# Kernel optimization log

Measured on AMD Instinct MI355X. Metric: run time of the kernel, lower is better.

## Reference

```python
import jax, jax.numpy as jnp
import numpy as np

N = 100000      # nodes
E = 1600000     # edges (avg degree 16)
NFEAT = 128
NHID = 128
NOUT = 1
BN_EPS = 1e-5


def setup_inputs() -> dict:
    key = jax.random.key(0)
    ks = jax.random.split(key, 8)
    s = 0.05  # weight scale for numerical stability through relu stack
    return {
        "x": jax.random.normal(ks[0], (N, NFEAT), jnp.float32),
        "edge_index": jax.random.randint(ks[1], (2, E), 0, N, dtype=jnp.int64),
        "edge_weight": jax.random.uniform(ks[2], (E,), jnp.float32),
        "conv1_W": jax.random.normal(ks[3], (NFEAT, NHID), jnp.float32) * s,
        "conv1_b": jnp.zeros((NHID,), jnp.float32),
        "conv2_W": jax.random.normal(ks[4], (NHID, NHID), jnp.float32) * s,
        "conv2_b": jnp.zeros((NHID,), jnp.float32),
        "bn1_gamma": jnp.ones((NHID,), jnp.float32),
        "bn1_beta": jnp.zeros((NHID,), jnp.float32),
        "bn2_gamma": jnp.ones((NHID,), jnp.float32),
        "bn2_beta": jnp.zeros((NHID,), jnp.float32),
        "fc1_W": jax.random.normal(ks[5], (NFEAT + 2 * NHID, NHID), jnp.float32) * s,
        "fc1_b": jnp.zeros((NHID,), jnp.float32),
        "fc2_W": jax.random.normal(ks[6], (NHID, NOUT), jnp.float32) * s,
        "fc2_b": jnp.zeros((NOUT,), jnp.float32),
    }


def _gcn_norm(edge_index, edge_weight, num_nodes):
    # PyG gcn_norm: add self-loops (weight 1), symmetric D^-1/2 A D^-1/2.
    row, col = edge_index[0], edge_index[1]
    loop = jnp.arange(num_nodes, dtype=row.dtype)
    rows = jnp.concatenate([row, loop])
    cols = jnp.concatenate([col, loop])
    w = jnp.concatenate([edge_weight, jnp.ones((num_nodes,), edge_weight.dtype)])
    deg = jax.ops.segment_sum(w, cols, num_segments=num_nodes)
    dinv = jnp.where(deg > 0, jax.lax.rsqrt(deg), 0.0)
    norm = dinv[rows] * w * dinv[cols]
    return rows, cols, norm


def _gcn_conv(x, rows, cols, norm, W, b, num_nodes):
    h = x @ W                                  # [N, out]
    msg = h[rows] * norm[:, None]              # gather + scale  [E+N, out]
    out = jax.ops.segment_sum(msg, cols, num_segments=num_nodes)  # scatter-add
    return out + b


def _bn(x, gamma, beta):
    # BatchNorm1d, training-mode batch statistics (biased variance)
    m = jnp.mean(x, axis=0)
    v = jnp.var(x, axis=0)
    return (x - m) * jax.lax.rsqrt(v + BN_EPS) * gamma + beta


def reference(x, edge_index, edge_weight, conv1_W, conv1_b, conv2_W, conv2_b,
              bn1_gamma, bn1_beta, bn2_gamma, bn2_beta,
              fc1_W, fc1_b, fc2_W, fc2_b):
    n = x.shape[0]
    rows, cols, norm = _gcn_norm(edge_index, edge_weight, n)
    h0 = x
    h1 = jax.nn.relu(_gcn_conv(h0, rows, cols, norm, conv1_W, conv1_b, n))
    h1 = _bn(h1, bn1_gamma, bn1_beta)          # dropout p=0 -> identity
    h2 = jax.nn.relu(_gcn_conv(h1, rows, cols, norm, conv2_W, conv2_b, n))
    h2 = _bn(h2, bn2_gamma, bn2_beta)
    cat = jnp.concatenate([h0, h1, h2], axis=1)   # [N, nfeat+2*nhid]
    z = jax.nn.relu(cat @ fc1_W + fc1_b)
    z = jax.nn.relu(z @ fc2_W + fc2_b)
    return z.reshape(-1)
```

## Files before the change

### kernel.cpp

```cpp
#include <hip/hip_runtime.h>

typedef __attribute__((ext_vector_type(8))) short short8;
typedef __attribute__((ext_vector_type(4))) float f32x4;

constexpr int N = 100000;
constexpr int E = 1600000;
constexpr int F = 128;
constexpr float EPS = 1e-5f;
constexpr int NB = (N + 1023) / 1024;

constexpr int R_RNG = 16;
constexpr int BINS = 6250;
constexpr int G2 = 64;
constexpr int NPB = 640;
constexpr int EPB = E / NPB;
constexpr int EPB4 = EPB / 4;

__device__ __forceinline__ short bf16hi(float v) {
  unsigned u = __float_as_uint(v);
  unsigned r = (u + 0x7fffu + ((u >> 16) & 1u)) >> 16;
  return (short)r;
}
__device__ __forceinline__ float bf16f(short h) {
  return __uint_as_float(((unsigned)(unsigned short)h) << 16);
}
__device__ __forceinline__ float bflo(unsigned v) {
  return __uint_as_float(v << 16);
}
__device__ __forceinline__ float bfhi(unsigned v) {
  return __uint_as_float(v & 0xffff0000u);
}

__global__ __launch_bounds__(256) void k_phist(const int* __restrict__ ei, int* __restrict__ Psl) {
  __shared__ int h16[16];
  const int b = blockIdx.x;
  const int tid = threadIdx.x;
  if (tid < 16) h16[tid] = 0;
  __syncthreads();
  const int4* cols4 = (const int4*)(ei + E);
  for (int t = tid; t < EPB4; t += 256) {
    int4 c = cols4[b * EPB4 + t];
    atomicAdd(&h16[c.x / BINS], 1);
    atomicAdd(&h16[c.y / BINS], 1);
    atomicAdd(&h16[c.z / BINS], 1);
    atomicAdd(&h16[c.w / BINS], 1);
  }
  __syncthreads();
  if (tid == 0) {
    int run = 0;
#pragma unroll
    for (int r = 0; r < 16; ++r) { Psl[b * 17 + r] = run; run += h16[r]; }
    Psl[b * 17 + 16] = run;
  }
}

__global__ __launch_bounds__(256) void k_pscatter(const int* __restrict__ ei, const float* __restrict__ ew,
                                                  const int* __restrict__ Psl, int2* __restrict__ pe) {
  __shared__ int cur[16];
  const int b = blockIdx.x;
  const int tid = threadIdx.x;
  if (tid < 16) cur[tid] = Psl[b * 17 + tid];
  __syncthreads();
  const int4* cols4 = (const int4*)(ei + E);
  const int4* rows4 = (const int4*)ei;
  const float4* ew4 = (const float4*)ew;
  const int base = b * EPB;
  for (int t = tid; t < EPB4; t += 256) {
    int4 c = cols4[b * EPB4 + t];
    int4 rr = rows4[b * EPB4 + t];
    float4 w = ew4[b * EPB4 + t];
#pragma unroll
    for (int j = 0; j < 4; ++j) {
      int cc = (j == 0) ? c.x : (j == 1) ? c.y : (j == 2) ? c.z : c.w;
      int rv = (j == 0) ? rr.x : (j == 1) ? rr.y : (j == 2) ? rr.z : rr.w;
      float wv = (j == 0) ? w.x : (j == 1) ? w.y : (j == 2) ? w.z : w.w;
      int r = cc / BINS;
      int pos = base + atomicAdd(&cur[r], 1);
      pe[pos] = make_int2((rv << 13) | (cc - r * BINS), __float_as_int(wv));
    }
  }
}

__global__ __launch_bounds__(256) void k_hist2(const int2* __restrict__ pe, const int* __restrict__ Psl,
                                               int* __restrict__ P) {
  __shared__ int hist[BINS];
  const int r = blockIdx.x / G2;
  const int g = blockIdx.x % G2;
  const int tid = threadIdx.x;
  for (int i = tid; i < BINS; i += 256) hist[i] = 0;
  __syncthreads();
  for (int b = g; b < NPB; b += G2) {
    const int s = Psl[b * 17 + r], e2 = Psl[b * 17 + r + 1];
    const int eb = b * EPB;
    for (int t = s + tid; t < e2; t += 256)
      atomicAdd(&hist[pe[eb + t].x & 0x1FFF], 1);
  }
  __syncthreads();
  for (int i = tid; i < BINS; i += 256) P[(size_t)blockIdx.x * BINS + i] = hist[i];
}

__global__ __launch_bounds__(256) void k_reduce(int* __restrict__ P, int* __restrict__ cnt) {
  int b = blockIdx.x * 256 + threadIdx.x;
  if (b >= N) return;
  int r = b / BINS, lb = b % BINS;
  size_t base = (size_t)r * G2 * BINS + lb;
  int run = 0;
#pragma unroll 4
  for (int g = 0; g < G2; ++g) {
    size_t idx = base + (size_t)g * BINS;
    int v = P[idx];
    P[idx] = run;
    run += v;
  }
  cnt[b] = run;
}

__global__ __launch_bounds__(256) void k_bsum(const int* __restrict__ cnt, int* __restrict__ bsum) {
  __shared__ int sh[256];
  int base = blockIdx.x * 1024 + threadIdx.x * 4;
  int s = 0;
  if (base + 3 < N) {
    int4 v = *(const int4*)&cnt[base];
    s = v.x + v.y + v.z + v.w;
  } else {
#pragma unroll
    for (int j = 0; j < 4; ++j)
      if (base + j < N) s += cnt[base + j];
  }
  sh[threadIdx.x] = s;
  __syncthreads();
  for (int o = 128; o > 0; o >>= 1) {
    if (threadIdx.x < o) sh[threadIdx.x] += sh[threadIdx.x + o];
    __syncthreads();
  }
  if (threadIdx.x == 0) bsum[blockIdx.x] = sh[0];
}

__global__ __launch_bounds__(128) void k_bscan(const int* __restrict__ bsum, int* __restrict__ bbase,
                                               int* __restrict__ offN) {
  __shared__ int sh[128];
  const int t = threadIdx.x;
  int v = (t < NB) ? bsum[t] : 0;
  sh[t] = v;
  __syncthreads();
  for (int o = 1; o < 128; o <<= 1) {
    int u = (t >= o) ? sh[t - o] : 0;
    __syncthreads();
    sh[t] += u;
    __syncthreads();
  }
  if (t < NB) bbase[t] = sh[t] - v;
  if (t == 127) *offN = sh[127];
}

__global__ __launch_bounds__(256) void k_off(const int* __restrict__ cnt, const int* __restrict__ bbase,
                                             int* __restrict__ off) {
  __shared__ int sh[256];
  int base = blockIdx.x * 1024 + threadIdx.x * 4;
  int c[4] = {0, 0, 0, 0};
  if (base + 3 < N) {
    int4 v = *(const int4*)&cnt[base];
    c[0] = v.x; c[1] = v.y; c[2] = v.z; c[3] = v.w;
  } else {
#pragma unroll
    for (int j = 0; j < 4; ++j)
      if (base + j < N) c[j] = cnt[base + j];
  }
  int s = c[0] + c[1] + c[2] + c[3];
  sh[threadIdx.x] = s;
  __syncthreads();
  for (int o = 1; o < 256; o <<= 1) {
    int u = (threadIdx.x >= o) ? sh[threadIdx.x - o] : 0;
    __syncthreads();
    sh[threadIdx.x] += u;
    __syncthreads();
  }
  int run = bbase[blockIdx.x] + sh[threadIdx.x] - s;
#pragma unroll
  for (int j = 0; j < 4; ++j) {
    if (base + j < N) { off[base + j] = run; run += c[j]; }
  }
}

__global__ __launch_bounds__(256) void k_scatter3(const int2* __restrict__ pe, const int* __restrict__ Psl,
                                                  const int* __restrict__ off, const int* __restrict__ P,
                                                  int2* __restrict__ cpair) {
  __shared__ int base[BINS];
  const int r = blockIdx.x / G2;
  const int g = blockIdx.x % G2;
  const int tid = threadIdx.x;
  for (int i = tid; i < BINS; i += 256)
    base[i] = off[r * BINS + i] + P[(size_t)blockIdx.x * BINS + i];
  __syncthreads();
  for (int b = g; b < NPB; b += G2) {
    const int s = Psl[b * 17 + r], e2 = Psl[b * 17 + r + 1];
    const int eb = b * EPB;
    for (int t = s + tid; t < e2; t += 256) {
      int2 p = pe[eb + t];
      int pos = atomicAdd(&base[p.x & 0x1FFF], 1);
      cpair[pos] = make_int2((int)(((unsigned)p.x) >> 13), p.y);
    }
  }
}

__global__ __launch_bounds__(256) void k_degcsc(const int2* __restrict__ cpair, const int* __restrict__ off,
                                                float* __restrict__ dinv) {
  int i = blockIdx.x * 256 + threadIdx.x;
  if (i >= N) return;
  int b = off[i], e2 = off[i + 1];
  float s = 1.0f;
  for (int p = b; p < e2; ++p) s += __int_as_float(cpair[p].y);
  dinv[i] = rsqrtf(s);
}

__global__ __launch_bounds__(256) void k_nrm(const int* __restrict__ off,
                                             const float* __restrict__ dinv, int2* __restrict__ cpair) {
  int i = blockIdx.x * 256 + threadIdx.x;
  if (i >= N) return;
  int b = off[i], e2 = off[i + 1];
  float di = dinv[i];
  for (int p = b; p < e2; ++p) {
    int2 cp = cpair[p];
    cpair[p].y = __float_as_int(dinv[cp.x] * __int_as_float(cp.y) * di);
  }
}

__global__ __launch_bounds__(256) void k_wprep_all(
    const float* __restrict__ W1, const float* __restrict__ W2, const float* __restrict__ Wf1,
    short* __restrict__ wt1h, short* __restrict__ wt1l,
    short* __restrict__ wt2h, short* __restrict__ wt2l,
    short* __restrict__ wtfh, short* __restrict__ wtfl,
    float* __restrict__ st1, float* __restrict__ st2) {
  int idx = blockIdx.x * 256 + threadIdx.x;
  if (idx < 256) st1[idx] = 0.f;
  else if (idx < 512) st2[idx - 256] = 0.f;
  const float* W;
  short *wh, *wl;
  int K, li;
  if (idx < 16384)      { W = W1;  wh = wt1h; wl = wt1l; K = 128; li = idx; }
  else if (idx < 32768) { W = W2;  wh = wt2h; wl = wt2l; K = 128; li = idx - 16384; }
  else if (idx < 81920) { W = Wf1; wh = wtfh; wl = wtfl; K = 384; li = idx - 32768; }
  else return;
  int k = li >> 7, c = li & 127;
  float v = W[(size_t)k * 128 + c];
  short h = bf16hi(v);
  short l = bf16hi(v - bf16f(h));
  wh[(size_t)c * K + k] = h;
  wl[(size_t)c * K + k] = l;
}

__global__ void k_bnparam(const float* __restrict__ st, const float* __restrict__ gamma,
                          const float* __restrict__ beta, float* __restrict__ p) {
  int t = threadIdx.x;
  if (t >= 128) return;
  const float inv_n = 1.0f / (float)N;
  float m = st[t] * inv_n;
  float var = fmaf(-m, m, st[128 + t] * inv_n);
  float sc = gamma[t] * rsqrtf(var + EPS);
  p[t] = sc;
  p[128 + t] = fmaf(-m, sc, beta[t]);
}

template <int KSTEPS, bool OBF16, bool FC2>
__global__ __launch_bounds__(256) void k_gemm_mfma(
    const float* __restrict__ a0, const float* __restrict__ p0,
    const float* __restrict__ a1, const float* __restrict__ p1,
    const float* __restrict__ a2, const float* __restrict__ p2,
    const short* __restrict__ wth, const short* __restrict__ wtl,
    const float* __restrict__ bias, void* __restrict__ Cout,
    const float* __restrict__ wf2, const float* __restrict__ bf2) {
  constexpr int KT = KSTEPS * 32;
  __shared__ short Ah[128][40];
  __shared__ short Al[128][40];
  __shared__ short Bh[128][40];
  __shared__ short Bl[128][40];
  __shared__ float red[2][128];

  const int tid = threadIdx.x;
  const int m0 = blockIdx.x * 128;
  const int sr = tid >> 1;
  const int sk = (tid & 1) * 16;
  const int arow = min(m0 + sr, N - 1);
  const int lane = tid & 63;
  const int lr = lane & 15;
  const int lg = lane >> 4;
  const int wv = tid >> 6;
  const int wr = wv >> 1;
  const int wc = wv & 1;

  f32x4 acc[4][4];
#pragma unroll
  for (int m = 0; m < 4; ++m)
#pragma unroll
    for (int n = 0; n < 4; ++n) acc[m][n] = (f32x4){0.f, 0.f, 0.f, 0.f};

  for (int ks = 0; ks < KSTEPS; ++ks) {
    const int seg = ks >> 2;
    const int koff = (ks & 3) * 32;
    const float* __restrict__ A = (seg == 0) ? a0 : ((seg == 1) ? a1 : a2);
    const float* __restrict__ P = (seg == 0) ? p0 : ((seg == 1) ? p1 : p2);

    const float4* src = (const float4*)(A + (size_t)arow * F + koff + sk);
    float v[16];
#pragma unroll
    for (int q = 0; q < 4; ++q) {
      float4 t = src[q];
      v[q * 4 + 0] = t.x; v[q * 4 + 1] = t.y; v[q * 4 + 2] = t.z; v[q * 4 + 3] = t.w;
    }
    if (P) {
      const int c0 = koff + sk;
#pragma unroll
      for (int q = 0; q < 4; ++q) {
        float4 s = *(const float4*)&P[c0 + q * 4];
        float4 b = *(const float4*)&P[128 + c0 + q * 4];
        v[q * 4 + 0] = fmaf(v[q * 4 + 0], s.x, b.x);
        v[q * 4 + 1] = fmaf(v[q * 4 + 1], s.y, b.y);
        v[q * 4 + 2] = fmaf(v[q * 4 + 2], s.z, b.z);
        v[q * 4 + 3] = fmaf(v[q * 4 + 3], s.w, b.w);
      }
    }
    short hh[16], ll[16];
#pragma unroll
    for (int j = 0; j < 16; ++j) {
      hh[j] = bf16hi(v[j]);
      ll[j] = bf16hi(v[j] - bf16f(hh[j]));
    }

    __syncthreads();

    short8 t0, t1, u0, u1;
#pragma unroll
    for (int j = 0; j < 8; ++j) { t0[j] = hh[j]; t1[j] = hh[8 + j]; u0[j] = ll[j]; u1[j] = ll[8 + j]; }
    *(short8*)&Ah[sr][sk] = t0;
    *(short8*)&Ah[sr][sk + 8] = t1;
    *(short8*)&Al[sr][sk] = u0;
    *(short8*)&Al[sr][sk + 8] = u1;

    const size_t wbase = (size_t)sr * KT + ks * 32 + sk;
    *(short8*)&Bh[sr][sk]     = *(const short8*)&wth[wbase];
    *(short8*)&Bh[sr][sk + 8] = *(const short8*)&wth[wbase + 8];
    *(short8*)&Bl[sr][sk]     = *(const short8*)&wtl[wbase];
    *(short8*)&Bl[sr][sk + 8] = *(const short8*)&wtl[wbase + 8];

    __syncthreads();

    short8 afh[4], afl[4], bfh[4], bfl[4];
#pragma unroll
    for (int m = 0; m < 4; ++m) {
      const int r2 = wr * 64 + m * 16 + lr;
      afh[m] = *(const short8*)&Ah[r2][lg * 8];
      afl[m] = *(const short8*)&Al[r2][lg * 8];
    }
#pragma unroll
    for (int n = 0; n < 4; ++n) {
      const int c2 = wc * 64 + n * 16 + lr;
      bfh[n] = *(const short8*)&Bh[c2][lg * 8];
      bfl[n] = *(const short8*)&Bl[c2][lg * 8];
    }
#pragma unroll
    for (int m = 0; m < 4; ++m)
#pragma unroll
      for (int n = 0; n < 4; ++n) {
        acc[m][n] = __builtin_amdgcn_mfma_f32_16x16x32_bf16(afh[m], bfh[n], acc[m][n], 0, 0, 0);
        acc[m][n] = __builtin_amdgcn_mfma_f32_16x16x32_bf16(afl[m], bfh[n], acc[m][n], 0, 0, 0);
        acc[m][n] = __builtin_amdgcn_mfma_f32_16x16x32_bf16(afh[m], bfl[n], acc[m][n], 0, 0, 0);
      }
  }

  float bv[4];
#pragma unroll
  for (int n = 0; n < 4; ++n) bv[n] = bias ? bias[wc * 64 + n * 16 + lr] : 0.f;

  if (FC2) {
    float w2v[4];
#pragma unroll
    for (int n = 0; n < 4; ++n) w2v[n] = wf2[wc * 64 + n * 16 + lr];
#pragma unroll
    for (int m = 0; m < 4; ++m) {
#pragma unroll
      for (int j = 0; j < 4; ++j) {
        float partial = 0.f;
#pragma unroll
        for (int n = 0; n < 4; ++n)
          partial += fmaxf(acc[m][n][j] + bv[n], 0.f) * w2v[n];
#pragma unroll
        for (int o = 8; o >= 1; o >>= 1) partial += __shfl_xor(partial, o, 16);
        if (lr == 0) red[wc][wr * 64 + m * 16 + lg * 4 + j] = partial;
      }
    }
    __syncthreads();
    if (tid < 128) {
      const int row = m0 + tid;
      if (row < N) {
        float s = red[0][tid] + red[1][tid] + bf2[0];
        ((float*)Cout)[row] = fmaxf(s, 0.f);
      }
    }
  } else {
#pragma unroll
    for (int m = 0; m < 4; ++m) {
#pragma unroll
      for (int j = 0; j < 4; ++j) {
        const int row = m0 + wr * 64 + m * 16 + lg * 4 + j;
        if (row < N) {
#pragma unroll
          for (int n = 0; n < 4; ++n) {
            const int col = wc * 64 + n * 16 + lr;
            float o = acc[m][n][j] + bv[n];
            if (bias) o = fmaxf(o, 0.f);
            if (OBF16) {
              ((unsigned short*)Cout)[(size_t)row * F + col] = (unsigned short)bf16hi(o);
            } else {
              ((float*)Cout)[(size_t)row * F + col] = o;
            }
          }
        }
      }
    }
  }
}

__global__ __launch_bounds__(256) void k_agg(
    const unsigned* __restrict__ h,
    const int2* __restrict__ cpair, const int* __restrict__ off,
    const float* __restrict__ dinv, const float* __restrict__ bias,
    float* __restrict__ out) {
  const int i = blockIdx.x * 4 + (threadIdx.x >> 6);
  if (i >= N) return;
  const int lane = threadIdx.x & 63;
  const float di = dinv[i];
  unsigned sv = h[(size_t)i * 64 + lane];
  float acc0 = di * di * bflo(sv);
  float acc1 = di * di * bfhi(sv);
  int e = off[i];
  const int eend = off[i + 1];
  for (; e + 8 <= eend; e += 8) {
    int2 cp[8];
    unsigned vv[8];
#pragma unroll
    for (int j = 0; j < 8; ++j) cp[j] = cpair[e + j];
#pragma unroll
    for (int j = 0; j < 8; ++j) vv[j] = h[(size_t)cp[j].x * 64 + lane];
#pragma unroll
    for (int j = 0; j < 8; ++j) {
      float w = __int_as_float(cp[j].y);
      acc0 = fmaf(w, bflo(vv[j]), acc0);
      acc1 = fmaf(w, bfhi(vv[j]), acc1);
    }
  }
  for (; e < eend; ++e) {
    int2 cp = cpair[e];
    float w = __int_as_float(cp.y);
    unsigned v = h[(size_t)cp.x * 64 + lane];
    acc0 = fmaf(w, bflo(v), acc0);
    acc1 = fmaf(w, bfhi(v), acc1);
  }
  float2 b = *(const float2*)&bias[lane * 2];
  float2 o = make_float2(fmaxf(acc0 + b.x, 0.f), fmaxf(acc1 + b.y, 0.f));
  *(float2*)&out[(size_t)i * F + lane * 2] = o;
}

__global__ __launch_bounds__(256) void k_stats(const float* __restrict__ h, float* __restrict__ sums) {
  const int col = threadIdx.x & 127;
  const int half = threadIdx.x >> 7;
  float s = 0.f, s2 = 0.f;
  for (int r = blockIdx.x * 2 + half; r < N; r += gridDim.x * 2) {
    float v = h[(size_t)r * F + col];
    s += v;
    s2 = fmaf(v, v, s2);
  }
  __shared__ float sh[256];
  sh[threadIdx.x] = s;
  __syncthreads();
  if (half == 0) atomicAdd(&sums[col], s + sh[col + 128]);
  __syncthreads();
  sh[threadIdx.x] = s2;
  __syncthreads();
  if (half == 0) atomicAdd(&sums[128 + col], s2 + sh[col + 128]);
}

extern "C" void kernel_launch(void* const* d_in, const int* in_sizes, int n_in,
                              void* d_out, int out_size, void* d_ws, size_t ws_size,
                              hipStream_t stream) {
  const float* x   = (const float*)d_in[0];
  const int*   ei  = (const int*)d_in[1];
  const float* ew  = (const float*)d_in[2];
  const float* W1  = (const float*)d_in[3];
  const float* b1  = (const float*)d_in[4];
  const float* W2  = (const float*)d_in[5];
  const float* b2  = (const float*)d_in[6];
  const float* g1  = (const float*)d_in[7];
  const float* be1 = (const float*)d_in[8];
  const float* g2  = (const float*)d_in[9];
  const float* be2 = (const float*)d_in[10];
  const float* Wf1 = (const float*)d_in[11];
  const float* bf1 = (const float*)d_in[12];
  const float* Wf2 = (const float*)d_in[13];
  const float* bf2 = (const float*)d_in[14];
  float* out = (float*)d_out;

  char* p = (char*)d_ws;
  auto take = [&](size_t bytes) {
    char* r = p;
    p += (bytes + 255) & ~(size_t)255;
    return r;
  };
  float* st1  = (float*)take(256 * 4);
  float* st2  = (float*)take(256 * 4);
  int*   cnt  = (int*)take((size_t)N * 4);
  int*   off  = (int*)take((size_t)(N + 1) * 4);
  int*   bsum = (int*)take((size_t)NB * 4);
  int*   bbase= (int*)take((size_t)NB * 4);
  int*   Psl  = (int*)take((size_t)NPB * 17 * 4);
  int2*  pe   = (int2*)take((size_t)E * 8);
  int*   Phist= (int*)take((size_t)R_RNG * G2 * BINS * 4);
  float* dinv = (float*)take((size_t)N * 4);
  float* p1   = (float*)take(256 * 4);
  float* p2   = (float*)take(256 * 4);
  short* wt1h = (short*)take((size_t)128 * 128 * 2);
  short* wt1l = (short*)take((size_t)128 * 128 * 2);
  short* wt2h = (short*)take((size_t)128 * 128 * 2);
  short* wt2l = (short*)take((size_t)128 * 128 * 2);
  short* wtfh = (short*)take((size_t)128 * 384 * 2);
  short* wtfl = (short*)take((size_t)128 * 384 * 2);
  int2*  cpair= (int2*)take((size_t)E * 8);
  unsigned short* bufH = (unsigned short*)take((size_t)N * F * 2);
  float* bufB = (float*)take((size_t)N * F * 4);
  float* bufC = (float*)take((size_t)N * F * 4);

  k_wprep_all<<<320, 256, 0, stream>>>(W1, W2, Wf1, wt1h, wt1l, wt2h, wt2l, wtfh, wtfl, st1, st2);

  k_phist<<<NPB, 256, 0, stream>>>(ei, Psl);
  k_pscatter<<<NPB, 256, 0, stream>>>(ei, ew, Psl, pe);
  k_hist2<<<R_RNG * G2, 256, 0, stream>>>(pe, Psl, Phist);
  k_reduce<<<(N + 255) / 256, 256, 0, stream>>>(Phist, cnt);
  k_bsum<<<NB, 256, 0, stream>>>(cnt, bsum);
  k_bscan<<<1, 128, 0, stream>>>(bsum, bbase, &off[N]);
  k_off<<<NB, 256, 0, stream>>>(cnt, bbase, off);
  k_scatter3<<<R_RNG * G2, 256, 0, stream>>>(pe, Psl, off, Phist, cpair);
  k_degcsc<<<(N + 255) / 256, 256, 0, stream>>>(cpair, off, dinv);
  k_nrm<<<(N + 255) / 256, 256, 0, stream>>>(off, dinv, cpair);

  const int gemm_grid = (N + 127) / 128;
  k_gemm_mfma<4, true, false><<<gemm_grid, 256, 0, stream>>>(
      x, nullptr, nullptr, nullptr, nullptr, nullptr, wt1h, wt1l, nullptr, bufH, nullptr, nullptr);
  k_agg<<<(N + 3) / 4, 256, 0, stream>>>((const unsigned*)bufH, cpair, off, dinv, b1, bufB);
  k_stats<<<256, 256, 0, stream>>>(bufB, st1);
  k_bnparam<<<1, 128, 0, stream>>>(st1, g1, be1, p1);
  k_gemm_mfma<4, true, false><<<gemm_grid, 256, 0, stream>>>(
      bufB, p1, nullptr, nullptr, nullptr, nullptr, wt2h, wt2l, nullptr, bufH, nullptr, nullptr);
  k_agg<<<(N + 3) / 4, 256, 0, stream>>>((const unsigned*)bufH, cpair, off, dinv, b2, bufC);
  k_stats<<<256, 256, 0, stream>>>(bufC, st2);
  k_bnparam<<<1, 128, 0, stream>>>(st2, g2, be2, p2);
  k_gemm_mfma<12, false, true><<<gemm_grid, 256, 0, stream>>>(
      x, nullptr, bufB, p1, bufC, p2, wtfh, wtfl, bf1, out, Wf2, bf2);
}
```

Measured before the change: 494.1 us.

## Store aggregated hidden activations as bf16 to halve intermediate traffic

The GCN aggregation outputs h1 and h2 are now written as packed bf16 pairs instead of fp32. The stats kernel and the downstream GEMMs read them through a new bf16 load path selected by a template mask. This halves the bytes written by aggregation and read by the stats and GEMM kernels, cutting memory traffic in several stages. In exchange the hidden activations lose precision, which feeds into the BatchNorm statistics and the final FC layer.

```diff
diff --git a/kernel.cpp b/kernel.cpp
--- a/kernel.cpp
+++ b/kernel.cpp
@@ -261,11 +261,11 @@
   p[128 + t] = fmaf(-m, sc, beta[t]);
 }
 
-template <int KSTEPS, bool OBF16, bool FC2>
+template <int KSTEPS, bool OBF16, bool FC2, int AMASK>
 __global__ __launch_bounds__(256) void k_gemm_mfma(
-    const float* __restrict__ a0, const float* __restrict__ p0,
-    const float* __restrict__ a1, const float* __restrict__ p1,
-    const float* __restrict__ a2, const float* __restrict__ p2,
+    const void* __restrict__ a0, const float* __restrict__ p0,
+    const void* __restrict__ a1, const float* __restrict__ p1,
+    const void* __restrict__ a2, const float* __restrict__ p2,
     const short* __restrict__ wth, const short* __restrict__ wtl,
     const float* __restrict__ bias, void* __restrict__ Cout,
     const float* __restrict__ wf2, const float* __restrict__ bf2) {
@@ -297,15 +297,29 @@
   for (int ks = 0; ks < KSTEPS; ++ks) {
     const int seg = ks >> 2;
     const int koff = (ks & 3) * 32;
-    const float* __restrict__ A = (seg == 0) ? a0 : ((seg == 1) ? a1 : a2);
+    const void* __restrict__ Av = (seg == 0) ? a0 : ((seg == 1) ? a1 : a2);
     const float* __restrict__ P = (seg == 0) ? p0 : ((seg == 1) ? p1 : p2);
-
-    const float4* src = (const float4*)(A + (size_t)arow * F + koff + sk);
+    const bool isbf = (AMASK >> seg) & 1;
+
     float v[16];
-#pragma unroll
-    for (int q = 0; q < 4; ++q) {
-      float4 t = src[q];
-      v[q * 4 + 0] = t.x; v[q * 4 + 1] = t.y; v[q * 4 + 2] = t.z; v[q * 4 + 3] = t.w;
+    if (isbf) {
+      const unsigned short* A16 = (const unsigned short*)Av;
+      const uint4* s16 = (const uint4*)&A16[(size_t)arow * F + koff + sk];
+      uint4 ua = s16[0], ub = s16[1];
+      unsigned uu[8] = {ua.x, ua.y, ua.z, ua.w, ub.x, ub.y, ub.z, ub.w};
+#pragma unroll
+      for (int j = 0; j < 8; ++j) {
+        v[2 * j] = bflo(uu[j]);
+        v[2 * j + 1] = bfhi(uu[j]);
+      }
+    } else {
+      const float* A = (const float*)Av;
+      const float4* src = (const float4*)(A + (size_t)arow * F + koff + sk);
+#pragma unroll
+      for (int q = 0; q < 4; ++q) {
+        float4 t = src[q];
+        v[q * 4 + 0] = t.x; v[q * 4 + 1] = t.y; v[q * 4 + 2] = t.z; v[q * 4 + 3] = t.w;
+      }
     }
     if (P) {
       const int c0 = koff + sk;
@@ -424,7 +438,7 @@
     const unsigned* __restrict__ h,
     const int2* __restrict__ cpair, const int* __restrict__ off,
     const float* __restrict__ dinv, const float* __restrict__ bias,
-    float* __restrict__ out) {
+    unsigned* __restrict__ out) {
   const int i = blockIdx.x * 4 + (threadIdx.x >> 6);
   if (i >= N) return;
   const int lane = threadIdx.x & 63;
@@ -456,27 +470,40 @@
     acc1 = fmaf(w, bfhi(v), acc1);
   }
   float2 b = *(const float2*)&bias[lane * 2];
-  float2 o = make_float2(fmaxf(acc0 + b.x, 0.f), fmaxf(acc1 + b.y, 0.f));
-  *(float2*)&out[(size_t)i * F + lane * 2] = o;
-}
-
-__global__ __launch_bounds__(256) void k_stats(const float* __restrict__ h, float* __restrict__ sums) {
-  const int col = threadIdx.x & 127;
-  const int half = threadIdx.x >> 7;
-  float s = 0.f, s2 = 0.f;
-  for (int r = blockIdx.x * 2 + half; r < N; r += gridDim.x * 2) {
-    float v = h[(size_t)r * F + col];
-    s += v;
-    s2 = fmaf(v, v, s2);
-  }
-  __shared__ float sh[256];
-  sh[threadIdx.x] = s;
-  __syncthreads();
-  if (half == 0) atomicAdd(&sums[col], s + sh[col + 128]);
-  __syncthreads();
-  sh[threadIdx.x] = s2;
-  __syncthreads();
-  if (half == 0) atomicAdd(&sums[128 + col], s2 + sh[col + 128]);
+  float o0 = fmaxf(acc0 + b.x, 0.f);
+  float o1 = fmaxf(acc1 + b.y, 0.f);
+  unsigned pack = ((unsigned)(unsigned short)bf16hi(o0)) |
+                  (((unsigned)(unsigned short)bf16hi(o1)) << 16);
+  out[(size_t)i * 64 + lane] = pack;
+}
+
+__global__ __launch_bounds__(256) void k_stats(const unsigned* __restrict__ h2, float* __restrict__ sums) {
+  const int cp = threadIdx.x & 63;
+  const int q = threadIdx.x >> 6;
+  float s0 = 0.f, s1 = 0.f, q0 = 0.f, q1 = 0.f;
+  for (int r = blockIdx.x * 4 + q; r < N; r += gridDim.x * 4) {
+    unsigned u = h2[(size_t)r * 64 + cp];
+    float lo = bflo(u), hi = bfhi(u);
+    s0 += lo; s1 += hi;
+    q0 = fmaf(lo, lo, q0);
+    q1 = fmaf(hi, hi, q1);
+  }
+  __shared__ float2 sh[256];
+  sh[threadIdx.x] = make_float2(s0, s1);
+  __syncthreads();
+  if (q == 0) {
+    float2 a = sh[cp], b = sh[64 + cp], c = sh[128 + cp], d = sh[192 + cp];
+    atomicAdd(&sums[2 * cp], a.x + b.x + c.x + d.x);
+    atomicAdd(&sums[2 * cp + 1], a.y + b.y + c.y + d.y);
+  }
+  __syncthreads();
+  sh[threadIdx.x] = make_float2(q0, q1);
+  __syncthreads();
+  if (q == 0) {
+    float2 a = sh[cp], b = sh[64 + cp], c = sh[128 + cp], d = sh[192 + cp];
+    atomicAdd(&sums[128 + 2 * cp], a.x + b.x + c.x + d.x);
+    atomicAdd(&sums[128 + 2 * cp + 1], a.y + b.y + c.y + d.y);
+  }
 }
 
 extern "C" void kernel_launch(void* const* d_in, const int* in_sizes, int n_in,
@@ -524,9 +551,9 @@
   short* wtfh = (short*)take((size_t)128 * 384 * 2);
   short* wtfl = (short*)take((size_t)128 * 384 * 2);
   int2*  cpair= (int2*)take((size_t)E * 8);
-  unsigned short* bufH = (unsigned short*)take((size_t)N * F * 2);
-  float* bufB = (float*)take((size_t)N * F * 4);
-  float* bufC = (float*)take((size_t)N * F * 4);
+  unsigned short* bufH  = (unsigned short*)take((size_t)N * F * 2);
+  unsigned short* bufB16= (unsigned short*)take((size_t)N * F * 2);
+  unsigned short* bufC16= (unsigned short*)take((size_t)N * F * 2);
 
   k_wprep_all<<<320, 256, 0, stream>>>(W1, W2, Wf1, wt1h, wt1l, wt2h, wt2l, wtfh, wtfl, st1, st2);
 
@@ -542,16 +569,18 @@
   k_nrm<<<(N + 255) / 256, 256, 0, stream>>>(off, dinv, cpair);
 
   const int gemm_grid = (N + 127) / 128;
-  k_gemm_mfma<4, true, false><<<gemm_grid, 256, 0, stream>>>(
+  k_gemm_mfma<4, true, false, 0><<<gemm_grid, 256, 0, stream>>>(
       x, nullptr, nullptr, nullptr, nullptr, nullptr, wt1h, wt1l, nullptr, bufH, nullptr, nullptr);
-  k_agg<<<(N + 3) / 4, 256, 0, stream>>>((const unsigned*)bufH, cpair, off, dinv, b1, bufB);
-  k_stats<<<256, 256, 0, stream>>>(bufB, st1);
+  k_agg<<<(N + 3) / 4, 256, 0, stream>>>((const unsigned*)bufH, cpair, off, dinv, b1,
+                                         (unsigned*)bufB16);
+  k_stats<<<256, 256, 0, stream>>>((const unsigned*)bufB16, st1);
   k_bnparam<<<1, 128, 0, stream>>>(st1, g1, be1, p1);
-  k_gemm_mfma<4, true, false><<<gemm_grid, 256, 0, stream>>>(
-      bufB, p1, nullptr, nullptr, nullptr, nullptr, wt2h, wt2l, nullptr, bufH, nullptr, nullptr);
-  k_agg<<<(N + 3) / 4, 256, 0, stream>>>((const unsigned*)bufH, cpair, off, dinv, b2, bufC);
-  k_stats<<<256, 256, 0, stream>>>(bufC, st2);
+  k_gemm_mfma<4, true, false, 1><<<gemm_grid, 256, 0, stream>>>(
+      bufB16, p1, nullptr, nullptr, nullptr, nullptr, wt2h, wt2l, nullptr, bufH, nullptr, nullptr);
+  k_agg<<<(N + 3) / 4, 256, 0, stream>>>((const unsigned*)bufH, cpair, off, dinv, b2,
+                                         (unsigned*)bufC16);
+  k_stats<<<256, 256, 0, stream>>>((const unsigned*)bufC16, st2);
   k_bnparam<<<1, 128, 0, stream>>>(st2, g2, be2, p2);
-  k_gemm_mfma<12, false, true><<<gemm_grid, 256, 0, stream>>>(
-      x, nullptr, bufB, p1, bufC, p2, wtfh, wtfl, bf1, out, Wf2, bf2);
-}
+  k_gemm_mfma<12, false, true, 6><<<gemm_grid, 256, 0, stream>>>(
+      x, nullptr, bufB16, p1, bufC16, p2, wtfh, wtfl, bf1, out, Wf2, bf2);
+}
```

After: 442.3 us. -10.5%, faster.
